# Kernel tuning notes

Measured on AMD Instinct MI355X. Metric: run time of the kernel, lower is better.

Reference implementation:

```python
import jax, jax.numpy as jnp
import numpy as np

B, C, H, W = 8, 256, 96, 96
HEADS, K = 8, 7  # kernel_size 7 -> 49 neighbors per query
HD = C // HEADS


def setup_inputs() -> dict:
    key = jax.random.key(0)
    ks = jax.random.split(key, 6)
    s = 0.02
    return {
        "x": jax.random.normal(ks[0], (B, C, H, W), jnp.float32),
        "wq": jax.random.normal(ks[1], (C, C), jnp.float32) * s,
        "wk": jax.random.normal(ks[2], (C, C), jnp.float32) * s,
        "wv": jax.random.normal(ks[3], (C, C), jnp.float32) * s,
        "w_proj": jax.random.normal(ks[4], (C, C), jnp.float32) * s,
        "b_proj": jnp.zeros((C,), jnp.float32),
        "rpb": jax.random.normal(ks[5], (HEADS, 2 * K - 1, 2 * K - 1), jnp.float32) * 0.02,
    }


def reference(x, wq, wk, wv, w_proj, b_proj, rpb):
    b, c, h, w = x.shape
    hd = c // HEADS
    scale = hd ** -0.5
    r = K // 2

    def conv1x1(wmat, t):
        return jnp.einsum('oc,bchw->bohw', wmat, t)

    def split_heads(t):
        # b (hd c) h w -> b hd h w c
        return t.reshape(b, HEADS, hd, h, w).transpose(0, 1, 3, 4, 2)

    q = split_heads(conv1x1(wq, x)) * scale
    k = split_heads(conv1x1(wk, x))
    v = split_heads(conv1x1(wv, x))

    # NATTEN neighborhood: window of size K starting at s_i, clamped to image
    s_h = jnp.clip(jnp.arange(h) - r, 0, h - K)  # (h,)
    s_w = jnp.clip(jnp.arange(w) - r, 0, w - K)  # (w,)
    off = jnp.arange(K)
    # relative-position-bias indices: (key_pos - query_pos) + (K-1) in [0, 2K-2]
    bi = s_h[:, None] + off[None, :] - jnp.arange(h)[:, None] + (K - 1)  # (h,K)
    bj = s_w[:, None] + off[None, :] - jnp.arange(w)[:, None] + (K - 1)  # (w,K)
    bias = rpb[:, bi[:, None, :, None], bj[None, :, None, :]]  # (heads,h,w,K,K)

    # QK: loop over the K*K fixed offsets (structural, not data-dim loop)
    logits = []
    for ki in range(K):
        k_r = k[:, :, s_h + ki]  # (b,heads,h,w,hd)
        for kj in range(K):
            k_sh = k_r[:, :, :, s_w + kj]
            logits.append(jnp.einsum('bhijc,bhijc->bhij', q, k_sh))
    attn = jnp.stack(logits, axis=-1).reshape(b, HEADS, h, w, K, K)
    attn = attn + bias[None]
    attn = jax.nn.softmax(attn.reshape(b, HEADS, h, w, K * K), axis=-1)
    attn = attn.reshape(b, HEADS, h, w, K, K)

    # AV: accumulate over the same offsets
    out = jnp.zeros_like(q)
    for ki in range(K):
        v_r = v[:, :, s_h + ki]
        for kj in range(K):
            v_sh = v_r[:, :, :, s_w + kj]
            out = out + attn[..., ki, kj, None] * v_sh

    # b hd h w f -> b h w (hd f), then proj (Linear dim->dim), back to b c h w
    merged = out.transpose(0, 2, 3, 1, 4).reshape(b, h, w, HEADS * hd)
    y = jnp.einsum('bhwc,oc->bhwo', merged, w_proj) + b_proj
    return y.transpose(0, 3, 1, 2)
```

## Files before the change

### kernel.cpp

```cpp
#include <hip/hip_runtime.h>
#include <stdint.h>

#define BATCH  8
#define CH     256
#define HH     96
#define WW     96
#define NHEADS 8
#define HD     32
#define KS     7
#define HWP    (HH*WW)
#define SCALE  0.17677669529663687f

#define HSTR  24
#define HSLOT 576
#define NT    11
#define PBS   200

typedef unsigned short ushort_t;
typedef unsigned short us8 __attribute__((ext_vector_type(8)));
typedef short s8v __attribute__((ext_vector_type(8)));
typedef float f4v __attribute__((ext_vector_type(4)));

__device__ __forceinline__ ushort_t f2bf(float f){
  unsigned int u = __float_as_uint(f);
  u = u + 0x7fffu + ((u >> 16) & 1u);
  return (ushort_t)(u >> 16);
}
__device__ __forceinline__ float bflo(unsigned int u){ return __uint_as_float(u << 16); }

__device__ __forceinline__ void gload_lds16(const void* g, void* l){
  __builtin_amdgcn_global_load_lds(
      (const __attribute__((address_space(1))) void*)g,
      (__attribute__((address_space(3))) void*)l, 16, 0, 0);
}

__global__ __launch_bounds__(256) void wcvt_kernel(
    const float* __restrict__ wq, const float* __restrict__ wk,
    const float* __restrict__ wv, const float* __restrict__ wp,
    ushort_t* __restrict__ wbf)
{
  int i = blockIdx.x*256 + threadIdx.x;
  int mat = i >> 16;
  int off = i & 65535;
  const float* src = (mat==0) ? wq : (mat==1) ? wk : (mat==2) ? wv : wp;
  wbf[i] = f2bf(src[off]);
}

__global__ __launch_bounds__(256) void xpose_kernel(
    const float* __restrict__ x, ushort_t* __restrict__ xT)
{
  __shared__ unsigned int tile[32][33];
  int p0 = blockIdx.x * 64;
  int c0 = blockIdx.y * 32;
  int b  = blockIdx.z;
  int tid = threadIdx.x;
  int tx = tid & 31, ty = tid >> 5;
  const float* xb = x + ((size_t)(b*CH + c0))*HWP;
  #pragma unroll
  for (int r = 0; r < 4; r++){
    int c = r*8 + ty;
    float2 v = *(const float2*)(xb + (size_t)c*HWP + p0 + tx*2);
    tile[c][tx] = (unsigned int)f2bf(v.x) | ((unsigned int)f2bf(v.y) << 16);
  }
  __syncthreads();
  int pv = tid >> 2, cq = tid & 3;
  ushort_t tmp[8];
  #pragma unroll
  for (int s = 0; s < 8; s++){
    unsigned int w = tile[cq*8 + s][pv >> 1];
    tmp[s] = (ushort_t)((pv & 1) ? (w >> 16) : (w & 0xffffu));
  }
  *(us8*)(xT + ((size_t)(b*HWP + p0 + pv))*CH + c0 + cq*8) = *(us8*)tmp;
}

__global__ __launch_bounds__(256) void qkv_gemm(
    const ushort_t* __restrict__ xT, const ushort_t* __restrict__ wbf,
    ushort_t* __restrict__ qb, ushort_t* __restrict__ kb, ushort_t* __restrict__ vb)
{
  __shared__ ushort_t As[128*32];
  __shared__ ushort_t Bs[128*32];
  int m0 = blockIdx.x * 128;
  int n0 = blockIdx.y * 128;
  int b  = blockIdx.z / 3;
  int mat= blockIdx.z % 3;
  int tid = threadIdx.x;
  int wave = tid >> 6, lane = tid & 63;
  const ushort_t* Abase = xT + ((size_t)(b*HWP + m0))*CH;
  const ushort_t* Bbase = wbf + mat*65536 + n0*CH;

  f4v acc[4][4];
  #pragma unroll
  for (int i=0;i<4;i++)
    #pragma unroll
    for (int j=0;j<4;j++) acc[i][j] = (f4v){0.f,0.f,0.f,0.f};

  int wm = wave & 1, wn = wave >> 1;
  int lane16 = lane & 15, quad = lane >> 4;
  int lrow = lane >> 2, lchunk = lane & 3;

  for (int kt = 0; kt < 8; kt++){
    #pragma unroll
    for (int inst = 0; inst < 2; inst++){
      int row0 = wave*32 + inst*16;
      gload_lds16(Abase + (size_t)(row0 + lrow)*CH + kt*32 + lchunk*8, &As[row0*32]);
      gload_lds16(Bbase + (size_t)(row0 + lrow)*CH + kt*32 + lchunk*8, &Bs[row0*32]);
    }
    __syncthreads();
    s8v a[4], bf[4];
    #pragma unroll
    for (int mi=0;mi<4;mi++) a[mi]  = *(const s8v*)&As[(wm*64 + mi*16 + lane16)*32 + quad*8];
    #pragma unroll
    for (int ni=0;ni<4;ni++) bf[ni] = *(const s8v*)&Bs[(wn*64 + ni*16 + lane16)*32 + quad*8];
    #pragma unroll
    for (int mi=0;mi<4;mi++)
      #pragma unroll
      for (int ni=0;ni<4;ni++)
        acc[mi][ni] = __builtin_amdgcn_mfma_f32_16x16x32_bf16(a[mi], bf[ni], acc[mi][ni], 0, 0, 0);
    __syncthreads();
  }

  ushort_t* dst = (mat==0) ? qb : (mat==1) ? kb : vb;
  float sc = (mat==0) ? SCALE : 1.0f;
  size_t obase = (size_t)b * NHEADS * HWP * HD;
  #pragma unroll
  for (int mi=0;mi<4;mi++){
    #pragma unroll
    for (int ni=0;ni<4;ni++){
      int o = n0 + wn*64 + ni*16 + lane16;
      int head = o >> 5, hd = o & 31;
      #pragma unroll
      for (int r=0;r<4;r++){
        int m = m0 + wm*64 + mi*16 + quad*4 + r;
        dst[obase + ((size_t)head*HWP + m)*HD + hd] = f2bf(acc[mi][ni][r] * sc);
      }
    }
  }
}

__global__ __launch_bounds__(256) void attn_kernel(
    const ushort_t* __restrict__ qb, const ushort_t* __restrict__ kb,
    const ushort_t* __restrict__ vb, const float* __restrict__ rpb,
    ushort_t* __restrict__ merged)
{
  __shared__ ushort_t kT[4*HSLOT*8];
  __shared__ ushort_t vTT[32*HSLOT];
  __shared__ ushort_t Pbuf[4][16*PBS];
  __shared__ float rpsPad[224];

  int tb = blockIdx.x;
  int i0 = (tb/6)*16, j0 = (tb%6)*16;
  int head = blockIdx.y, b = blockIdx.z;
  int tid = threadIdx.x;
  int wave = tid >> 6, lane = tid & 63;
  int lane16 = lane & 15, quad = lane >> 4;

  int hs0 = max(i0-3, 0);
  int ws0 = max(j0-3, 0);
  size_t kvbase = ((size_t)(b*NHEADS + head)) * HWP * HD;

  for (int pb = wave; pb < 9; pb += 4){
    int s = pb*64 + lane;
    int xx = s >> 3; int r = (xx*171) >> 9;
    int c24 = s - r*24; int cc = min(c24, 21);
    int gr = min(hs0 + r,  HH-1);
    int gc = min(ws0 + cc, WW-1);
    const ushort_t* gp = kb + kvbase + (size_t)(gr*WW + gc)*HD;
    #pragma unroll
    for (int c = 0; c < 4; c++)
      gload_lds16(gp + c*8, &kT[c*(HSLOT*8) + pb*64*8]);
  }
  for (int it = 0; it < 9; it++){
    int idx = it*256 + tid;
    int pix = idx >> 2, c = idx & 3;
    int xx = pix >> 3; int r = (xx*171) >> 9;
    int c24 = pix - r*24; int cc = min(c24, 21);
    int gr = min(hs0 + r,  HH-1);
    int gc = min(ws0 + cc, WW-1);
    us8 vv = *(const us8*)(vb + kvbase + (size_t)(gr*WW + gc)*HD + c*8);
    #pragma unroll
    for (int e = 0; e < 8; e++) vTT[(c*8+e)*HSLOT + pix] = vv[e];
  }
  if (tid < 224) rpsPad[tid] = (tid >= 16 && tid < 185) ? rpb[head*169 + tid - 16] : 0.f;

  s8v qfrag[4];
  #pragma unroll
  for (int rr = 0; rr < 4; rr++){
    int i = i0 + wave*4 + rr;
    qfrag[rr] = *(const s8v*)(qb + kvbase + (size_t)(i*WW + j0 + lane16)*HD + quad*8);
  }

  unsigned int pk[22];
  #pragma unroll
  for (int ii = 0; ii < 22; ii++){
    unsigned int w = 0;
    #pragma unroll
    for (int h = 0; h < 2; h++){
      int idx = ii*2 + h;
      int tt = idx >> 2, r = idx & 3;
      int n = tt*16 + quad*4 + r;
      int xx = n >> 3; int rk = (xx*171) >> 9;
      int col = n - rk*24;
      int code = (rk >= 7) ? 255 : col;
      int m13c = rk*13 + col;
      w |= (unsigned)((code & 255) | (m13c << 8)) << (h*16);
    }
    pk[ii] = w;
  }

  int j = j0 + lane16;
  int cs_g = min(max(j-3, 0), WW-KS);
  unsigned int cs = (unsigned)(cs_g - ws0);
  int lanePart = ws0 - j + 6 + 16;

  __syncthreads();

  #pragma unroll 1
  for (int rr = 0; rr < 4; rr++){
    int i = i0 + wave*4 + rr;
    int si_g = min(max(i-3, 0), HH-KS);
    int si = si_g - hs0;
    int bi0 = si_g - i + 6;
    int rowBase = bi0*13 + lanePart;
    int kbase = si*HSTR;

    f4v c[NT];
    #pragma unroll
    for (int tt = 0; tt < NT; tt++){
      s8v af = *(const s8v*)&kT[quad*(HSLOT*8) + (kbase + tt*16 + lane16)*8];
      c[tt] = __builtin_amdgcn_mfma_f32_16x16x32_bf16(af, qfrag[rr], (f4v){0.f,0.f,0.f,0.f}, 0, 0, 0);
    }

    float s = 0.f;
    #pragma unroll
    for (int tt = 0; tt < NT; tt++){
      #pragma unroll
      for (int r = 0; r < 4; r++){
        int idx = tt*4 + r;
        unsigned int ex = pk[idx >> 1] >> ((idx & 1)*16);
        unsigned int col = ex & 255u;
        int m13c = (int)((ex >> 8) & 255u);
        float bias = rpsPad[rowBase + m13c];
        float e = __expf(c[tt][r] + bias);
        e = ((col - cs) <= 6u) ? e : 0.f;
        s += e;
        c[tt][r] = e;
      }
    }
    s += __shfl_xor(s, 16);
    s += __shfl_xor(s, 32);
    float inv = 1.0f / s;

    ushort_t* pw = &Pbuf[wave][lane16*PBS];
    #pragma unroll
    for (int tt = 0; tt < NT; tt++){
      uint2 pp;
      pp.x = (unsigned)f2bf(c[tt][0]*inv) | ((unsigned)f2bf(c[tt][1]*inv) << 16);
      pp.y = (unsigned)f2bf(c[tt][2]*inv) | ((unsigned)f2bf(c[tt][3]*inv) << 16);
      *(uint2*)&pw[tt*16 + quad*4] = pp;
    }
    *(uint2*)&pw[NT*16 + quad*4] = (uint2){0u, 0u};

    f4v o0 = {0.f,0.f,0.f,0.f}, o1 = {0.f,0.f,0.f,0.f};
    #pragma unroll
    for (int kk = 0; kk < 6; kk++){
      s8v pa = *(const s8v*)&Pbuf[wave][lane16*PBS + kk*32 + quad*8];
      s8v v0 = *(const s8v*)&vTT[lane16*HSLOT      + kbase + kk*32 + quad*8];
      s8v v1 = *(const s8v*)&vTT[(16+lane16)*HSLOT + kbase + kk*32 + quad*8];
      o0 = __builtin_amdgcn_mfma_f32_16x16x32_bf16(pa, v0, o0, 0, 0, 0);
      o1 = __builtin_amdgcn_mfma_f32_16x16x32_bf16(pa, v1, o1, 0, 0, 0);
    }

    size_t mb = ((size_t)(b*HWP) + (size_t)i*WW + j0 + quad*4)*CH + head*HD + lane16;
    #pragma unroll
    for (int r = 0; r < 4; r++){
      merged[mb + (size_t)r*CH]      = f2bf(o0[r]);
      merged[mb + (size_t)r*CH + 16] = f2bf(o1[r]);
    }
  }
}

__global__ __launch_bounds__(256) void proj_gemm(
    const ushort_t* __restrict__ merged, const ushort_t* __restrict__ wbf,
    const float* __restrict__ bias, float* __restrict__ y)
{
  __shared__ ushort_t As[128*32];
  __shared__ ushort_t Bs[128*32];
  int m0 = blockIdx.x * 128;
  int n0 = blockIdx.y * 128;
  int b  = blockIdx.z;
  int tid = threadIdx.x;
  int wave = tid >> 6, lane = tid & 63;
  const ushort_t* Abase = merged + ((size_t)(b*HWP + m0))*CH;
  const ushort_t* Bbase = wbf + 3*65536 + n0*CH;

  f4v acc[4][4];
  #pragma unroll
  for (int i=0;i<4;i++)
    #pragma unroll
    for (int j=0;j<4;j++) acc[i][j] = (f4v){0.f,0.f,0.f,0.f};

  int wm = wave & 1, wn = wave >> 1;
  int lane16 = lane & 15, quad = lane >> 4;
  int lrow = lane >> 2, lchunk = lane & 3;

  for (int kt = 0; kt < 8; kt++){
    #pragma unroll
    for (int inst = 0; inst < 2; inst++){
      int row0 = wave*32 + inst*16;
      gload_lds16(Abase + (size_t)(row0 + lrow)*CH + kt*32 + lchunk*8, &As[row0*32]);
      gload_lds16(Bbase + (size_t)(row0 + lrow)*CH + kt*32 + lchunk*8, &Bs[row0*32]);
    }
    __syncthreads();
    s8v a[4], bf[4];
    #pragma unroll
    for (int mi=0;mi<4;mi++) a[mi]  = *(const s8v*)&As[(wm*64 + mi*16 + lane16)*32 + quad*8];
    #pragma unroll
    for (int ni=0;ni<4;ni++) bf[ni] = *(const s8v*)&Bs[(wn*64 + ni*16 + lane16)*32 + quad*8];
    #pragma unroll
    for (int mi=0;mi<4;mi++)
      #pragma unroll
      for (int ni=0;ni<4;ni++)
        acc[mi][ni] = __builtin_amdgcn_mfma_f32_16x16x32_bf16(a[mi], bf[ni], acc[mi][ni], 0, 0, 0);
    __syncthreads();
  }

  #pragma unroll
  for (int mi=0;mi<4;mi++){
    #pragma unroll
    for (int ni=0;ni<4;ni++){
      int o = n0 + wn*64 + ni*16 + lane16;
      float bo = bias[o];
      int mb = m0 + wm*64 + mi*16 + quad*4;
      float4 val;
      val.x = acc[mi][ni][0] + bo;
      val.y = acc[mi][ni][1] + bo;
      val.z = acc[mi][ni][2] + bo;
      val.w = acc[mi][ni][3] + bo;
      *(float4*)&y[((size_t)(b*CH + o))*HWP + mb] = val;
    }
  }
}

extern "C" void kernel_launch(void* const* d_in, const int* in_sizes, int n_in,
                              void* d_out, int out_size, void* d_ws, size_t ws_size,
                              hipStream_t stream)
{
  const float* x   = (const float*)d_in[0];
  const float* wq  = (const float*)d_in[1];
  const float* wk  = (const float*)d_in[2];
  const float* wv  = (const float*)d_in[3];
  const float* wp  = (const float*)d_in[4];
  const float* bp  = (const float*)d_in[5];
  const float* rpb = (const float*)d_in[6];
  float* y = (float*)d_out;

  const size_t SZ = (size_t)BATCH * HWP * CH * 2;
  char* ws = (char*)d_ws;
  ushort_t* xT     = (ushort_t*)ws;  ws += SZ;
  ushort_t* qbuf   = (ushort_t*)ws;  ws += SZ;
  ushort_t* kbuf   = (ushort_t*)ws;  ws += SZ;
  ushort_t* vbuf   = (ushort_t*)ws;  ws += SZ;
  ushort_t* merged = (ushort_t*)ws;  ws += SZ;
  ushort_t* wbf    = (ushort_t*)ws;  ws += (size_t)4*65536*2;
  if (ws_size < (size_t)5*SZ + 4*65536*2) return;

  wcvt_kernel <<<dim3(1024),        dim3(256), 0, stream>>>(wq, wk, wv, wp, wbf);
  xpose_kernel<<<dim3(144, 8, 8),   dim3(256), 0, stream>>>(x, xT);
  qkv_gemm    <<<dim3(72, 2, 24),   dim3(256), 0, stream>>>(xT, wbf, qbuf, kbuf, vbuf);
  attn_kernel <<<dim3(36, 8, 8),    dim3(256), 0, stream>>>(qbuf, kbuf, vbuf, rpb, merged);
  proj_gemm   <<<dim3(72, 2, 8),    dim3(256), 0, stream>>>(merged, wbf, bp, y);
}
```

Before: 383.0 us.

## Use 8 waves per attention block, two query rows per wave, pad V tile stride

The attention kernel now runs 512 threads per block, so each wave handles two query rows instead of four. Each wave issues both rows' QK MFMAs and softmax together for more instruction-level parallelism, then runs AV sequentially through a shared P buffer. The V transposed tile stride is padded from 576 to 584 to reduce LDS bank conflicts. The cost is more register pressure (two sets of 11 accumulators) and a larger per-block LDS footprint from the doubled P buffers, which may limit occupancy.

```diff
diff --git a/kernel.cpp b/kernel.cpp
--- a/kernel.cpp
+++ b/kernel.cpp
@@ -13,6 +13,7 @@
 
 #define HSTR  24
 #define HSLOT 576
+#define VSTR  584
 #define NT    11
 #define PBS   200
 
@@ -137,14 +138,14 @@
   }
 }
 
-__global__ __launch_bounds__(256) void attn_kernel(
+__global__ __launch_bounds__(512) void attn_kernel(
     const ushort_t* __restrict__ qb, const ushort_t* __restrict__ kb,
     const ushort_t* __restrict__ vb, const float* __restrict__ rpb,
     ushort_t* __restrict__ merged)
 {
   __shared__ ushort_t kT[4*HSLOT*8];
-  __shared__ ushort_t vTT[32*HSLOT];
-  __shared__ ushort_t Pbuf[4][16*PBS];
+  __shared__ ushort_t vTT[32*VSTR];
+  __shared__ ushort_t Pbuf[8][16*PBS];
   __shared__ float rpsPad[224];
 
   int tb = blockIdx.x;
@@ -158,7 +159,7 @@
   int ws0 = max(j0-3, 0);
   size_t kvbase = ((size_t)(b*NHEADS + head)) * HWP * HD;
 
-  for (int pb = wave; pb < 9; pb += 4){
+  for (int pb = wave; pb < 9; pb += 8){
     int s = pb*64 + lane;
     int xx = s >> 3; int r = (xx*171) >> 9;
     int c24 = s - r*24; int cc = min(c24, 21);
@@ -169,25 +170,24 @@
     for (int c = 0; c < 4; c++)
       gload_lds16(gp + c*8, &kT[c*(HSLOT*8) + pb*64*8]);
   }
-  for (int it = 0; it < 9; it++){
-    int idx = it*256 + tid;
-    int pix = idx >> 2, c = idx & 3;
-    int xx = pix >> 3; int r = (xx*171) >> 9;
-    int c24 = pix - r*24; int cc = min(c24, 21);
-    int gr = min(hs0 + r,  HH-1);
-    int gc = min(ws0 + cc, WW-1);
-    us8 vv = *(const us8*)(vb + kvbase + (size_t)(gr*WW + gc)*HD + c*8);
-    #pragma unroll
-    for (int e = 0; e < 8; e++) vTT[(c*8+e)*HSLOT + pix] = vv[e];
+  #pragma unroll
+  for (int it = 0; it < 5; it++){
+    int idx = it*512 + tid;
+    if (idx < 2304){
+      int pix = idx >> 2, c = idx & 3;
+      int xx = pix >> 3; int r = (xx*171) >> 9;
+      int c24 = pix - r*24; int cc = min(c24, 21);
+      int gr = min(hs0 + r,  HH-1);
+      int gc = min(ws0 + cc, WW-1);
+      us8 vv = *(const us8*)(vb + kvbase + (size_t)(gr*WW + gc)*HD + c*8);
+      #pragma unroll
+      for (int e = 0; e < 8; e++) vTT[(c*8+e)*VSTR + pix] = vv[e];
+    }
   }
   if (tid < 224) rpsPad[tid] = (tid >= 16 && tid < 185) ? rpb[head*169 + tid - 16] : 0.f;
 
-  s8v qfrag[4];
-  #pragma unroll
-  for (int rr = 0; rr < 4; rr++){
-    int i = i0 + wave*4 + rr;
-    qfrag[rr] = *(const s8v*)(qb + kvbase + (size_t)(i*WW + j0 + lane16)*HD + quad*8);
-  }
+  s8v qfragA = *(const s8v*)(qb + kvbase + (size_t)((i0 + wave*2    )*WW + j0 + lane16)*HD + quad*8);
+  s8v qfragB = *(const s8v*)(qb + kvbase + (size_t)((i0 + wave*2 + 1)*WW + j0 + lane16)*HD + quad*8);
 
   unsigned int pk[22];
   #pragma unroll
@@ -214,67 +214,101 @@
 
   __syncthreads();
 
-  #pragma unroll 1
-  for (int rr = 0; rr < 4; rr++){
-    int i = i0 + wave*4 + rr;
-    int si_g = min(max(i-3, 0), HH-KS);
-    int si = si_g - hs0;
-    int bi0 = si_g - i + 6;
-    int rowBase = bi0*13 + lanePart;
-    int kbase = si*HSTR;
-
-    f4v c[NT];
-    #pragma unroll
-    for (int tt = 0; tt < NT; tt++){
-      s8v af = *(const s8v*)&kT[quad*(HSLOT*8) + (kbase + tt*16 + lane16)*8];
-      c[tt] = __builtin_amdgcn_mfma_f32_16x16x32_bf16(af, qfrag[rr], (f4v){0.f,0.f,0.f,0.f}, 0, 0, 0);
-    }
-
-    float s = 0.f;
-    #pragma unroll
-    for (int tt = 0; tt < NT; tt++){
-      #pragma unroll
-      for (int r = 0; r < 4; r++){
-        int idx = tt*4 + r;
-        unsigned int ex = pk[idx >> 1] >> ((idx & 1)*16);
-        unsigned int col = ex & 255u;
-        int m13c = (int)((ex >> 8) & 255u);
-        float bias = rpsPad[rowBase + m13c];
-        float e = __expf(c[tt][r] + bias);
-        e = ((col - cs) <= 6u) ? e : 0.f;
-        s += e;
-        c[tt][r] = e;
-      }
-    }
-    s += __shfl_xor(s, 16);
-    s += __shfl_xor(s, 32);
-    float inv = 1.0f / s;
-
-    ushort_t* pw = &Pbuf[wave][lane16*PBS];
-    #pragma unroll
-    for (int tt = 0; tt < NT; tt++){
-      uint2 pp;
-      pp.x = (unsigned)f2bf(c[tt][0]*inv) | ((unsigned)f2bf(c[tt][1]*inv) << 16);
-      pp.y = (unsigned)f2bf(c[tt][2]*inv) | ((unsigned)f2bf(c[tt][3]*inv) << 16);
-      *(uint2*)&pw[tt*16 + quad*4] = pp;
-    }
-    *(uint2*)&pw[NT*16 + quad*4] = (uint2){0u, 0u};
-
-    f4v o0 = {0.f,0.f,0.f,0.f}, o1 = {0.f,0.f,0.f,0.f};
-    #pragma unroll
-    for (int kk = 0; kk < 6; kk++){
-      s8v pa = *(const s8v*)&Pbuf[wave][lane16*PBS + kk*32 + quad*8];
-      s8v v0 = *(const s8v*)&vTT[lane16*HSLOT      + kbase + kk*32 + quad*8];
-      s8v v1 = *(const s8v*)&vTT[(16+lane16)*HSLOT + kbase + kk*32 + quad*8];
-      o0 = __builtin_amdgcn_mfma_f32_16x16x32_bf16(pa, v0, o0, 0, 0, 0);
-      o1 = __builtin_amdgcn_mfma_f32_16x16x32_bf16(pa, v1, o1, 0, 0, 0);
-    }
-
-    size_t mb = ((size_t)(b*HWP) + (size_t)i*WW + j0 + quad*4)*CH + head*HD + lane16;
+  int iA = i0 + wave*2, iB = iA + 1;
+  int siA_g = min(max(iA-3, 0), HH-KS);
+  int siB_g = min(max(iB-3, 0), HH-KS);
+  int rowBaseA = (siA_g - iA + 6)*13 + lanePart;
+  int rowBaseB = (siB_g - iB + 6)*13 + lanePart;
+  int kbaseA = (siA_g - hs0)*HSTR;
+  int kbaseB = (siB_g - hs0)*HSTR;
+
+  f4v cA[NT], cB[NT];
+  #pragma unroll
+  for (int tt = 0; tt < NT; tt++){
+    s8v af = *(const s8v*)&kT[quad*(HSLOT*8) + (kbaseA + tt*16 + lane16)*8];
+    cA[tt] = __builtin_amdgcn_mfma_f32_16x16x32_bf16(af, qfragA, (f4v){0.f,0.f,0.f,0.f}, 0, 0, 0);
+  }
+  #pragma unroll
+  for (int tt = 0; tt < NT; tt++){
+    s8v af = *(const s8v*)&kT[quad*(HSLOT*8) + (kbaseB + tt*16 + lane16)*8];
+    cB[tt] = __builtin_amdgcn_mfma_f32_16x16x32_bf16(af, qfragB, (f4v){0.f,0.f,0.f,0.f}, 0, 0, 0);
+  }
+
+  float sA = 0.f, sB = 0.f;
+  #pragma unroll
+  for (int tt = 0; tt < NT; tt++){
+    #pragma unroll
+    for (int r = 0; r < 4; r++){
+      int idx = tt*4 + r;
+      unsigned int ex = pk[idx >> 1] >> ((idx & 1)*16);
+      unsigned int col = ex & 255u;
+      int m13c = (int)((ex >> 8) & 255u);
+      float eA = __expf(cA[tt][r] + rpsPad[rowBaseA + m13c]);
+      float eB = __expf(cB[tt][r] + rpsPad[rowBaseB + m13c]);
+      bool valid = ((col - cs) <= 6u);
+      eA = valid ? eA : 0.f;
+      eB = valid ? eB : 0.f;
+      sA += eA; sB += eB;
+      cA[tt][r] = eA; cB[tt][r] = eB;
+    }
+  }
+  sA += __shfl_xor(sA, 16); sA += __shfl_xor(sA, 32);
+  sB += __shfl_xor(sB, 16); sB += __shfl_xor(sB, 32);
+  float invA = 1.0f / sA, invB = 1.0f / sB;
+
+  ushort_t* pw = &Pbuf[wave][lane16*PBS];
+
+  #pragma unroll
+  for (int tt = 0; tt < NT; tt++){
+    uint2 pp;
+    pp.x = (unsigned)f2bf(cA[tt][0]*invA) | ((unsigned)f2bf(cA[tt][1]*invA) << 16);
+    pp.y = (unsigned)f2bf(cA[tt][2]*invA) | ((unsigned)f2bf(cA[tt][3]*invA) << 16);
+    *(uint2*)&pw[tt*16 + quad*4] = pp;
+  }
+  *(uint2*)&pw[NT*16 + quad*4] = (uint2){0u, 0u};
+
+  f4v o0 = {0.f,0.f,0.f,0.f}, o1 = {0.f,0.f,0.f,0.f};
+  #pragma unroll
+  for (int kk = 0; kk < 6; kk++){
+    s8v pa = *(const s8v*)&Pbuf[wave][lane16*PBS + kk*32 + quad*8];
+    s8v v0 = *(const s8v*)&vTT[lane16*VSTR      + kbaseA + kk*32 + quad*8];
+    s8v v1 = *(const s8v*)&vTT[(16+lane16)*VSTR + kbaseA + kk*32 + quad*8];
+    o0 = __builtin_amdgcn_mfma_f32_16x16x32_bf16(pa, v0, o0, 0, 0, 0);
+    o1 = __builtin_amdgcn_mfma_f32_16x16x32_bf16(pa, v1, o1, 0, 0, 0);
+  }
+  {
+    size_t mb = ((size_t)(b*HWP) + (size_t)iA*WW + j0 + quad*4)*CH + head*HD + lane16;
     #pragma unroll
     for (int r = 0; r < 4; r++){
       merged[mb + (size_t)r*CH]      = f2bf(o0[r]);
       merged[mb + (size_t)r*CH + 16] = f2bf(o1[r]);
+    }
+  }
+
+  #pragma unroll
+  for (int tt = 0; tt < NT; tt++){
+    uint2 pp;
+    pp.x = (unsigned)f2bf(cB[tt][0]*invB) | ((unsigned)f2bf(cB[tt][1]*invB) << 16);
+    pp.y = (unsigned)f2bf(cB[tt][2]*invB) | ((unsigned)f2bf(cB[tt][3]*invB) << 16);
+    *(uint2*)&pw[tt*16 + quad*4] = pp;
+  }
+  *(uint2*)&pw[NT*16 + quad*4] = (uint2){0u, 0u};
+
+  f4v p0 = {0.f,0.f,0.f,0.f}, p1 = {0.f,0.f,0.f,0.f};
+  #pragma unroll
+  for (int kk = 0; kk < 6; kk++){
+    s8v pa = *(const s8v*)&Pbuf[wave][lane16*PBS + kk*32 + quad*8];
+    s8v v0 = *(const s8v*)&vTT[lane16*VSTR      + kbaseB + kk*32 + quad*8];
+    s8v v1 = *(const s8v*)&vTT[(16+lane16)*VSTR + kbaseB + kk*32 + quad*8];
+    p0 = __builtin_amdgcn_mfma_f32_16x16x32_bf16(pa, v0, p0, 0, 0, 0);
+    p1 = __builtin_amdgcn_mfma_f32_16x16x32_bf16(pa, v1, p1, 0, 0, 0);
+  }
+  {
+    size_t mb = ((size_t)(b*HWP) + (size_t)iB*WW + j0 + quad*4)*CH + head*HD + lane16;
+    #pragma unroll
+    for (int r = 0; r < 4; r++){
+      merged[mb + (size_t)r*CH]      = f2bf(p0[r]);
+      merged[mb + (size_t)r*CH + 16] = f2bf(p1[r]);
     }
   }
 }
@@ -367,6 +401,6 @@
   wcvt_kernel <<<dim3(1024),        dim3(256), 0, stream>>>(wq, wk, wv, wp, wbf);
   xpose_kernel<<<dim3(144, 8, 8),   dim3(256), 0, stream>>>(x, xT);
   qkv_gemm    <<<dim3(72, 2, 24),   dim3(256), 0, stream>>>(xT, wbf, qbuf, kbuf, vbuf);
-  attn_kernel <<<dim3(36, 8, 8),    dim3(256), 0, stream>>>(qbuf, kbuf, vbuf, rpb, merged);
+  attn_kernel <<<dim3(36, 8, 8),    dim3(512), 0, stream>>>(qbuf, kbuf, vbuf, rpb, merged);
   proj_gemm   <<<dim3(72, 2, 8),    dim3(256), 0, stream>>>(merged, wbf, bp, y);
 }
```

Result: faster. 311.9 us (-18.6%).
